# Kernel tuning notes

Measured on AMD Instinct MI355X. Metric: run time of the kernel, lower is better.

## Reference

```python
import jax, jax.numpy as jnp
import numpy as np

# PairwiseChannelAdd(aggregation='max', mode='off-diag', source_axis=1)
# For each source channel k in [0, C-2]:
#   right = x[:, k+1:] + x[:, k];  left = x[:, :k+1] + x[:, k]
#   union of right+left covers ALL j in [0, C-1] (diagonal j==k included via `left`).
#   connec_k = max over (pair axis j, time axis T) of (x[:, j] + x[:, k])  -> [B, 1, F]
# stack over k -> [C-1, B, 1, F]; transpose([1,2,0,3]) -> [B, 1, C-1, F]

B, C, T, F = 8, 160, 512, 32

def setup_inputs() -> dict:
    key = jax.random.key(0)
    x = jax.random.normal(key, (B, C, T, F), dtype=jnp.float32)
    return {"x": x}

def reference(x):
    c = x.shape[1]
    ks = jnp.arange(c - 1)
    # lax.map keeps memory at one [B,C,T,F] pairwise-sum intermediate per step
    def per_k(k):
        # x[:, k] -> [B, T, F]; broadcast-add against all channels j -> [B, C, T, F]
        s = x + x[:, k][:, None, :, :]
        return jnp.max(s, axis=(1, 2))  # reduce over pair (j) and time -> [B, F]
    out = jax.lax.map(per_k, ks)        # [C-1, B, F]
    return jnp.transpose(out, (1, 0, 2))[:, None, :, :]  # [B, 1, C-1, F]
```

## Files before the change

kernel.cpp:

```cpp
#include <hip/hip_runtime.h>
#include <math.h>

#define B_DIM 8
#define C_DIM 160
#define T_DIM 512
#define F_DIM 32
#define F4 8
#define C1 159
#define TC 8
#define NT (T_DIM / TC)

__device__ __forceinline__ float4 fmax4(float4 a, float4 b) {
    return make_float4(fmaxf(a.x, b.x), fmaxf(a.y, b.y),
                       fmaxf(a.z, b.z), fmaxf(a.w, b.w));
}
__device__ __forceinline__ float4 fadd4(float4 a, float4 b) {
    return make_float4(a.x + b.x, a.y + b.y, a.z + b.z, a.w + b.w);
}
__device__ __forceinline__ float4 shfl_xor4(float4 v, int m) {
    return make_float4(__shfl_xor(v.x, m), __shfl_xor(v.y, m),
                       __shfl_xor(v.z, m), __shfl_xor(v.w, m));
}
#define NEG_INF4 make_float4(-INFINITY, -INFINITY, -INFINITY, -INFINITY)

__global__ __launch_bounds__(256)
void fused_kernel(const float* __restrict__ x, float* __restrict__ partial) {
    const int blk = blockIdx.x;
    const int b = blk >> 6;
    const int tc = blk & (NT - 1);
    const int t_base = tc * TC;
    const int tid = threadIdx.x;
    const int f4 = tid & 7;

    const float4* __restrict__ x4 = (const float4*)x;
    float4* __restrict__ p4 = (float4*)partial;

    __shared__ float4 red[256];
    __shared__ float4 Mlds[TC * F4];

    {
        const int tl = (tid >> 3) & 7;
        const int cs = tid >> 6;
        const int base = (b * C_DIM * T_DIM + (t_base + tl)) * F4 + f4;
        float4 acc = NEG_INF4;
        #pragma unroll 8
        for (int i = 0; i < 40; ++i) {
            const int c = i * 4 + cs;
            acc = fmax4(acc, x4[base + c * (T_DIM * F4)]);
        }
        red[tid] = acc;
        __syncthreads();
        if (tid < 128) red[tid] = fmax4(red[tid], red[tid + 128]);
        __syncthreads();
        if (tid < 64) Mlds[tid] = fmax4(red[tid], red[tid + 64]);
        __syncthreads();
    }

    {
        const int kg = tid >> 3;
        float4 m[TC];
        #pragma unroll
        for (int tl = 0; tl < TC; ++tl) m[tl] = Mlds[tl * 8 + f4];

        #pragma unroll
        for (int ki = 0; ki < 5; ++ki) {
            const int k = kg + 32 * ki;
            if (k < C1) {
                const float4* __restrict__ xk =
                    x4 + ((b * C_DIM + k) * T_DIM + t_base) * F4 + f4;
                float4 acc = NEG_INF4;
                #pragma unroll
                for (int tl = 0; tl < TC; ++tl)
                    acc = fmax4(acc, fadd4(xk[tl * F4], m[tl]));
                p4[((b * C1 + k) * NT + tc) * F4 + f4] = acc;
            }
        }
    }
}

__global__ __launch_bounds__(64)
void combine_kernel(const float* __restrict__ partial, float* __restrict__ out) {
    const int bk = blockIdx.x;
    const int lane = threadIdx.x;
    const float4* __restrict__ p = (const float4*)partial + bk * (NT * F4);

    float4 acc = NEG_INF4;
    #pragma unroll
    for (int j = 0; j < (NT * F4) / 64; ++j)
        acc = fmax4(acc, p[j * 64 + lane]);

    acc = fmax4(acc, shfl_xor4(acc, 8));
    acc = fmax4(acc, shfl_xor4(acc, 16));
    acc = fmax4(acc, shfl_xor4(acc, 32));
    if (lane < 8)
        ((float4*)out)[bk * F4 + lane] = acc;
}

extern "C" void kernel_launch(void* const* d_in, const int* in_sizes, int n_in,
                              void* d_out, int out_size, void* d_ws, size_t ws_size,
                              hipStream_t stream) {
    const float* x = (const float*)d_in[0];
    float* out = (float*)d_out;
    float* partial = (float*)d_ws;

    fused_kernel<<<B_DIM * NT, 256, 0, stream>>>(x, partial);
    combine_kernel<<<B_DIM * C1, 64, 0, stream>>>(partial, out);
}
```

Measured before the change: 128.1 us.

## Stage x tile in LDS to avoid reading global memory twice

The fused kernel now loads each 2-timestep slice of x once into padded shared memory. It computes the per-time channel max with shuffles plus a small cross-wave LDS reduction, then reads the k rows back from LDS instead of reloading them from global memory. It loops over four sub-chunks and keeps the accumulators in registers. This roughly halves global reads of x, at the cost of about 43KB of LDS per block (lower occupancy) and extra barriers per sub-chunk.

```diff
diff --git a/kernel.cpp b/kernel.cpp
--- a/kernel.cpp
+++ b/kernel.cpp
@@ -7,8 +7,10 @@
 #define F_DIM 32
 #define F4 8
 #define C1 159
-#define TC 8
-#define NT (T_DIM / TC)
+#define TCH 8
+#define NT (T_DIM / TCH)
+#define NSUB 4
+#define KPAD 17
 
 __device__ __forceinline__ float4 fmax4(float4 a, float4 b) {
     return make_float4(fmaxf(a.x, b.x), fmaxf(a.y, b.y),
@@ -28,53 +30,63 @@
     const int blk = blockIdx.x;
     const int b = blk >> 6;
     const int tc = blk & (NT - 1);
-    const int t_base = tc * TC;
+    const int t_base = tc * TCH;
     const int tid = threadIdx.x;
     const int f4 = tid & 7;
+    const int eid = tid & 15;
+    const int cg = tid >> 4;
+    const int wave = tid >> 6;
 
     const float4* __restrict__ x4 = (const float4*)x;
     float4* __restrict__ p4 = (float4*)partial;
 
-    __shared__ float4 red[256];
-    __shared__ float4 Mlds[TC * F4];
+    __shared__ float4 Xlds[C_DIM * KPAD];
+    __shared__ float4 redw[4 * 16];
 
-    {
-        const int tl = (tid >> 3) & 7;
-        const int cs = tid >> 6;
-        const int base = (b * C_DIM * T_DIM + (t_base + tl)) * F4 + f4;
-        float4 acc = NEG_INF4;
-        #pragma unroll 8
-        for (int i = 0; i < 40; ++i) {
-            const int c = i * 4 + cs;
-            acc = fmax4(acc, x4[base + c * (T_DIM * F4)]);
+    const int kg = tid >> 3;
+    float4 accK[5];
+    #pragma unroll
+    for (int ki = 0; ki < 5; ++ki) accK[ki] = NEG_INF4;
+
+    for (int s = 0; s < NSUB; ++s) {
+        const int t0 = t_base + 2 * s;
+
+        float4 macc = NEG_INF4;
+        #pragma unroll
+        for (int i = 0; i < 10; ++i) {
+            const int c = cg + 16 * i;
+            const float4 v = x4[((b * C_DIM + c) * T_DIM + t0) * F4 + eid];
+            Xlds[c * KPAD + eid] = v;
+            macc = fmax4(macc, v);
         }
-        red[tid] = acc;
+        macc = fmax4(macc, shfl_xor4(macc, 16));
+        macc = fmax4(macc, shfl_xor4(macc, 32));
+        if ((tid & 63) < 16) redw[wave * 16 + eid] = macc;
         __syncthreads();
-        if (tid < 128) red[tid] = fmax4(red[tid], red[tid + 128]);
-        __syncthreads();
-        if (tid < 64) Mlds[tid] = fmax4(red[tid], red[tid + 64]);
-        __syncthreads();
-    }
 
-    {
-        const int kg = tid >> 3;
-        float4 m[TC];
-        #pragma unroll
-        for (int tl = 0; tl < TC; ++tl) m[tl] = Mlds[tl * 8 + f4];
+        float4 m0 = fmax4(fmax4(redw[f4],      redw[16 + f4]),
+                          fmax4(redw[32 + f4], redw[48 + f4]));
+        float4 m1 = fmax4(fmax4(redw[8 + f4],      redw[16 + 8 + f4]),
+                          fmax4(redw[32 + 8 + f4], redw[48 + 8 + f4]));
 
         #pragma unroll
         for (int ki = 0; ki < 5; ++ki) {
             const int k = kg + 32 * ki;
             if (k < C1) {
-                const float4* __restrict__ xk =
-                    x4 + ((b * C_DIM + k) * T_DIM + t_base) * F4 + f4;
-                float4 acc = NEG_INF4;
-                #pragma unroll
-                for (int tl = 0; tl < TC; ++tl)
-                    acc = fmax4(acc, fadd4(xk[tl * F4], m[tl]));
-                p4[((b * C1 + k) * NT + tc) * F4 + f4] = acc;
+                accK[ki] = fmax4(accK[ki],
+                                 fadd4(Xlds[k * KPAD + f4], m0));
+                accK[ki] = fmax4(accK[ki],
+                                 fadd4(Xlds[k * KPAD + 8 + f4], m1));
             }
         }
+        __syncthreads();
+    }
+
+    #pragma unroll
+    for (int ki = 0; ki < 5; ++ki) {
+        const int k = kg + 32 * ki;
+        if (k < C1)
+            p4[((b * C1 + k) * NT + tc) * F4 + f4] = accK[ki];
     }
 }
 
```

New measurement: 120.5 us. -5.9%, faster.
